# Kernel tuning notes

Measured on AMD Instinct MI355X. Metric: run time of the kernel, lower is better.

Reference implementation:

```python
import jax, jax.numpy as jnp
import numpy as np

TAU_U = 1.0
TAU_L = 0.05
EPS = 1e-12  # torch F.normalize eps


def setup_inputs() -> dict:
    key = jax.random.key(0)
    ks = jax.random.split(key, 8)
    N, D, B = 100000, 128, 8192
    x1 = jax.random.normal(ks[0], (N, D), dtype=jnp.float32)
    x2 = jax.random.normal(ks[1], (N, D), dtype=jnp.float32)
    x1_index = jax.random.randint(ks[2], (B,), 0, N, dtype=jnp.int64 if jax.config.jax_enable_x64 else jnp.int32)
    x2_index = jax.random.randint(ks[3], (B,), 0, N, dtype=jnp.int64 if jax.config.jax_enable_x64 else jnp.int32)
    # Linear params (torch Linear default init: U(-1/sqrt(fan_in), 1/sqrt(fan_in)))
    lim1 = 1.0 / np.sqrt(D)
    W1 = jax.random.uniform(ks[4], (D, D), minval=-lim1, maxval=lim1, dtype=jnp.float32)
    b1 = jax.random.uniform(ks[5], (D,), minval=-lim1, maxval=lim1, dtype=jnp.float32)
    W2 = jax.random.uniform(ks[6], (1, D), minval=-lim1, maxval=lim1, dtype=jnp.float32)
    b2 = jax.random.uniform(ks[7], (1,), minval=-lim1, maxval=lim1, dtype=jnp.float32)
    return {"x1": x1, "x2": x2, "x1_index": x1_index, "x2_index": x2_index,
            "W1": W1, "b1": b1, "W2": W2, "b2": b2}


def _l2norm(x):
    # matches torch F.normalize(dim=1) for 2-D input
    n = jnp.sqrt(jnp.sum(x * x, axis=-1, keepdims=True))
    return x / jnp.maximum(n, EPS)


def reference(x1, x2, x1_index, x2_index, W1, b1, W2, b2):
    x1_feat = _l2norm(x1[x1_index])          # [B, D]
    x2_feat = _l2norm(x2[x2_index])          # [B, D]

    h = x1_feat * x2_feat                    # [B, D]
    h = h @ W1.T + b1                        # lin1
    h = jnp.where(h >= 0, h, 0.2 * h)        # leaky_relu(0.2)
    s = jax.nn.sigmoid(h @ W2.T + b2)        # [B, 1]
    ssl_temp = (TAU_U - TAU_L) * (1.0 - s) + TAU_L   # [B, 1]

    pos = jnp.sum(x1_feat * x2_feat, axis=-1)         # [B]
    # NOTE: [B] / [B,1] broadcasts to [B,B] exactly like torch
    pos_rating = jnp.exp(pos / ssl_temp)              # [B, B]

    tot = x1_feat @ x2_feat.T                          # [B, B]
    tot_rating = jnp.sum(jnp.exp(tot / ssl_temp), axis=1)  # [B]

    ssl_temp_avg = jnp.mean(ssl_temp)
    return (pos_rating, tot_rating, ssl_temp_avg)
```

## Files before the change

kernel.cpp:

```cpp
#include <hip/hip_runtime.h>
#include <stdint.h>

typedef __bf16 bf16x8 __attribute__((ext_vector_type(8)));
typedef float f32x4 __attribute__((ext_vector_type(4)));
typedef __attribute__((address_space(3))) uint32_t as3u32;
typedef const __attribute__((address_space(1))) uint32_t as1u32;

#define B_TOT 8192
#define DD 128
#define OUT_TOT 67108864UL
#define OUT_AVG 67117056UL

__device__ inline unsigned short f2bf(float x){
  union { float f; uint32_t u; } v; v.f = x;
  return (unsigned short)((v.u + 0x7fffu + ((v.u >> 16) & 1u)) >> 16);
}

__device__ inline float bsum128(float v, volatile float* s2){
  #pragma unroll
  for (int o = 32; o; o >>= 1) v += __shfl_xor(v, o);
  __syncthreads();
  if ((threadIdx.x & 63) == 0) s2[threadIdx.x >> 6] = v;
  __syncthreads();
  return s2[0] + s2[1];
}

__global__ __launch_bounds__(128) void k_feat(const float* __restrict__ x1,
    const float* __restrict__ x2, const int* __restrict__ i1a, const int* __restrict__ i2a,
    unsigned short* __restrict__ f1b, unsigned short* __restrict__ f2b,
    unsigned short* __restrict__ hb, float* __restrict__ posw){
  __shared__ float s2[2];
  int b = blockIdx.x, t = threadIdx.x;
  size_t r1 = (size_t)i1a[b] * DD, r2 = (size_t)i2a[b] * DD;
  float v1 = x1[r1 + t], v2 = x2[r2 + t];
  float n1 = sqrtf(bsum128(v1 * v1, s2));
  float f1 = v1 / fmaxf(n1, 1e-12f);
  float n2 = sqrtf(bsum128(v2 * v2, s2));
  float f2 = v2 / fmaxf(n2, 1e-12f);
  float h = f1 * f2;
  float pos = bsum128(h, s2);
  int o = b * DD + t;
  f1b[o] = f2bf(f1); f2b[o] = f2bf(f2); hb[o] = f2bf(h);
  if (t == 0) posw[b] = pos;
}

__device__ inline void stage_tile(const unsigned short* g, unsigned short* s){
  int tid = threadIdx.x;
  #pragma unroll
  for (int it = 0; it < 8; ++it){
    int c = tid + it * 256;
    int row = c >> 4, cc = c & 15;
    int src = (row << 4) + (cc ^ (row & 7));
    __builtin_amdgcn_global_load_lds((as1u32*)(g + src * 8),
                                     (as3u32*)(s + c * 8), 16, 0, 0);
  }
}

__device__ inline void mfma_tile(const unsigned short* As, const unsigned short* Bs,
                                 f32x4 acc[4][4]){
  int tid = threadIdx.x;
  int w = tid >> 6, l = tid & 63;
  int wr = (w >> 1) * 64, wc = (w & 1) * 64;
  int lo = l & 15, hi = l >> 4;
  f32x4 zero = {0.f, 0.f, 0.f, 0.f};
  #pragma unroll
  for (int m = 0; m < 4; ++m)
    #pragma unroll
    for (int n = 0; n < 4; ++n) acc[m][n] = zero;
  #pragma unroll
  for (int kk = 0; kk < 4; ++kk){
    bf16x8 af[4], bfv[4];
    #pragma unroll
    for (int m = 0; m < 4; ++m){
      int row = wr + m * 16 + lo;
      af[m] = *(const bf16x8*)(As + row * 128 + ((kk * 4 + hi) ^ (row & 7)) * 8);
    }
    #pragma unroll
    for (int n = 0; n < 4; ++n){
      int row = wc + n * 16 + lo;
      bfv[n] = *(const bf16x8*)(Bs + row * 128 + ((kk * 4 + hi) ^ (row & 7)) * 8);
    }
    #pragma unroll
    for (int m = 0; m < 4; ++m)
      #pragma unroll
      for (int n = 0; n < 4; ++n)
        acc[m][n] = __builtin_amdgcn_mfma_f32_16x16x32_bf16(af[m], bfv[n], acc[m][n], 0, 0, 0);
  }
}

__global__ __launch_bounds__(256) void k_lin(const unsigned short* __restrict__ hb,
    const float* __restrict__ W1, const float* __restrict__ b1,
    const float* __restrict__ W2, const float* __restrict__ b2,
    float* __restrict__ Tw, float* __restrict__ rTw, float* __restrict__ Tpart){
  __shared__ __align__(16) unsigned short As[16384];
  __shared__ __align__(16) unsigned short Bs[16384];
  __shared__ float zpart[2][128];
  __shared__ float s4[4];
  int i0 = blockIdx.x * 128;
  int tid = threadIdx.x;
  stage_tile(hb + (size_t)i0 * 128, As);
  #pragma unroll
  for (int it = 0; it < 8; ++it){
    int c = tid + it * 256;
    int row = c >> 4, cc = c & 15;
    int src = (row << 4) + (cc ^ (row & 7));
    const float4* g4 = (const float4*)(W1 + src * 8);
    float4 a = g4[0], b = g4[1];
    unsigned short t8[8];
    t8[0] = f2bf(a.x); t8[1] = f2bf(a.y); t8[2] = f2bf(a.z); t8[3] = f2bf(a.w);
    t8[4] = f2bf(b.x); t8[5] = f2bf(b.y); t8[6] = f2bf(b.z); t8[7] = f2bf(b.w);
    *(uint4*)(Bs + c * 8) = *(uint4*)t8;
  }
  asm volatile("s_waitcnt vmcnt(0)" ::: "memory");
  __syncthreads();
  f32x4 acc[4][4];
  mfma_tile(As, Bs, acc);
  int w = tid >> 6, l = tid & 63;
  int wrb = (w >> 1) * 64, wcb = (w & 1) * 64, lo = l & 15, hi = l >> 4;
  float w2v[4], b1v[4];
  #pragma unroll
  for (int n = 0; n < 4; ++n){ int col = wcb + n * 16 + lo; w2v[n] = W2[col]; b1v[n] = b1[col]; }
  #pragma unroll
  for (int m = 0; m < 4; ++m){
    #pragma unroll
    for (int q = 0; q < 4; ++q){
      float p = 0.f;
      #pragma unroll
      for (int n = 0; n < 4; ++n){
        float hv = acc[m][n][q] + b1v[n];
        hv = hv >= 0.f ? hv : 0.2f * hv;
        p += hv * w2v[n];
      }
      p += __shfl_xor(p, 1); p += __shfl_xor(p, 2);
      p += __shfl_xor(p, 4); p += __shfl_xor(p, 8);
      if (lo == 0) zpart[w & 1][wrb + m * 16 + hi * 4 + q] = p;
    }
  }
  __syncthreads();
  float Tloc = 0.f;
  if (tid < 128){
    float z = zpart[0][tid] + zpart[1][tid] + b2[0];
    float s = 1.f / (1.f + __expf(-z));
    float T = 0.95f * (1.f - s) + 0.05f;
    Tw[i0 + tid] = T; rTw[i0 + tid] = 1.f / T;
    Tloc = T;
  }
  float v = Tloc;
  #pragma unroll
  for (int o = 32; o; o >>= 1) v += __shfl_xor(v, o);
  if ((tid & 63) == 0) s4[tid >> 6] = v;
  __syncthreads();
  if (tid == 0) Tpart[blockIdx.x] = s4[0] + s4[1] + s4[2] + s4[3];
}

__global__ __launch_bounds__(256) void k_tot(const unsigned short* __restrict__ f1b,
    const unsigned short* __restrict__ f2b, const float* __restrict__ rTw,
    const float* __restrict__ posw, float* __restrict__ totpart,
    float* __restrict__ out){
  __shared__ __align__(16) unsigned short As[16384];
  __shared__ __align__(16) unsigned short Bs[16384];
  __shared__ float rowacc[2][128];
  __shared__ float posS[128];
  __shared__ float rS[128];
  int bx = (blockIdx.x & 7) * 512 + (blockIdx.x >> 3);
  int rt = bx >> 6, ct = bx & 63;
  stage_tile(f1b + (size_t)rt * 16384, As);
  stage_tile(f2b + (size_t)ct * 16384, Bs);
  asm volatile("s_waitcnt vmcnt(0)" ::: "memory");
  __syncthreads();
  f32x4 acc[4][4];
  mfma_tile(As, Bs, acc);
  int tid = threadIdx.x, w = tid >> 6, l = tid & 63;
  int wrb = (w >> 1) * 64, lo = l & 15, hi = l >> 4;
  int i0 = rt * 128;
  if (tid < 128) posS[tid] = posw[ct * 128 + tid];
  else           rS[tid - 128] = rTw[i0 + tid - 128];
  #pragma unroll
  for (int m = 0; m < 4; ++m){
    #pragma unroll
    for (int q = 0; q < 4; ++q){
      int lr = wrb + m * 16 + hi * 4 + q;
      float r = rTw[i0 + lr];
      float p = __expf(acc[m][0][q] * r) + __expf(acc[m][1][q] * r)
              + __expf(acc[m][2][q] * r) + __expf(acc[m][3][q] * r);
      p += __shfl_xor(p, 1); p += __shfl_xor(p, 2);
      p += __shfl_xor(p, 4); p += __shfl_xor(p, 8);
      if (lo == 0) rowacc[w & 1][lr] = p;
    }
  }
  __syncthreads();
  if (tid < 128) totpart[(size_t)ct * B_TOT + i0 + tid] = rowacc[0][tid] + rowacc[1][tid];
  int c0 = (tid & 31) * 4;
  f32x4 p4 = *(const f32x4*)&posS[c0];
  #pragma unroll
  for (int pass = 0; pass < 16; ++pass){
    int row = pass * 8 + (tid >> 5);
    float r = rS[row];
    f32x4 e;
    e.x = __expf(p4.x * r); e.y = __expf(p4.y * r);
    e.z = __expf(p4.z * r); e.w = __expf(p4.w * r);
    __builtin_nontemporal_store(e, (f32x4*)(out + (size_t)(i0 + row) * B_TOT + ct * 128 + c0));
  }
}

__global__ __launch_bounds__(256) void k_red(const float* __restrict__ totpart,
    const float* __restrict__ Tpart, float* __restrict__ out){
  int i = blockIdx.x * 256 + threadIdx.x;
  float s = 0.f;
  #pragma unroll 8
  for (int ct = 0; ct < 64; ++ct) s += totpart[(size_t)ct * B_TOT + i];
  out[OUT_TOT + i] = s;
  if (blockIdx.x == 0 && threadIdx.x < 64){
    float v = Tpart[threadIdx.x];
    #pragma unroll
    for (int o = 32; o; o >>= 1) v += __shfl_xor(v, o);
    if (threadIdx.x == 0) out[OUT_AVG] = v * (1.0f / 8192.0f);
  }
}

extern "C" void kernel_launch(void* const* d_in, const int* in_sizes, int n_in,
                              void* d_out, int out_size, void* d_ws, size_t ws_size,
                              hipStream_t stream){
  const float* x1 = (const float*)d_in[0];
  const float* x2 = (const float*)d_in[1];
  const int*   i1 = (const int*)d_in[2];
  const int*   i2 = (const int*)d_in[3];
  const float* W1 = (const float*)d_in[4];
  const float* b1 = (const float*)d_in[5];
  const float* W2 = (const float*)d_in[6];
  const float* b2 = (const float*)d_in[7];
  float* out = (float*)d_out;
  char* ws = (char*)d_ws;
  unsigned short* hb   = (unsigned short*)(ws);
  unsigned short* f1b  = (unsigned short*)(ws + 2097152);
  unsigned short* f2b  = (unsigned short*)(ws + 4194304);
  float* posw  = (float*)(ws + 6291456);
  float* Tw    = (float*)(ws + 6324224);
  float* rTw   = (float*)(ws + 6356992);
  float* Tpart = (float*)(ws + 6389760);
  float* totpart = (float*)(ws + 6390016);

  hipLaunchKernelGGL(k_feat,  dim3(8192), dim3(128), 0, stream, x1, x2, i1, i2, f1b, f2b, hb, posw);
  hipLaunchKernelGGL(k_lin,   dim3(64),   dim3(256), 0, stream, hb, W1, b1, W2, b2, Tw, rTw, Tpart);
  hipLaunchKernelGGL(k_tot,   dim3(4096), dim3(256), 0, stream, f1b, f2b, rTw, posw, totpart, out);
  hipLaunchKernelGGL(k_red,   dim3(32),   dim3(256), 0, stream, totpart, Tpart, out);
}
```

Baseline: 100.8 us.

## Replace reduction kernel with atomics and read A fragments directly from global

Removes the final reduction kernel. Row sums of exp(tot/T) are now accumulated into the output with atomicAdd from each tile, and the temperature mean is accumulated atomically from k_lin. The output accumulators are zeroed in k_feat. k_tot no longer stages the A tile into LDS: it loads A fragments straight from global memory, which halves LDS use, and it sets launch bounds to allow 4 blocks per CU. In exchange there are 64 atomic adds per output row, float sums become order-nondeterministic, and the A fragment loads are uncoalesced global reads.

```diff
diff --git a/kernel.cpp b/kernel.cpp
--- a/kernel.cpp
+++ b/kernel.cpp
@@ -28,9 +28,11 @@
 __global__ __launch_bounds__(128) void k_feat(const float* __restrict__ x1,
     const float* __restrict__ x2, const int* __restrict__ i1a, const int* __restrict__ i2a,
     unsigned short* __restrict__ f1b, unsigned short* __restrict__ f2b,
-    unsigned short* __restrict__ hb, float* __restrict__ posw){
+    unsigned short* __restrict__ hb, float* __restrict__ posw, float* __restrict__ out){
   __shared__ float s2[2];
   int b = blockIdx.x, t = threadIdx.x;
+  int gid = b * 128 + t;
+  if (gid <= 8192) out[OUT_TOT + gid] = 0.f;
   size_t r1 = (size_t)i1a[b] * DD, r2 = (size_t)i2a[b] * DD;
   float v1 = x1[r1 + t], v2 = x2[r2 + t];
   float n1 = sqrtf(bsum128(v1 * v1, s2));
@@ -91,7 +93,7 @@
 __global__ __launch_bounds__(256) void k_lin(const unsigned short* __restrict__ hb,
     const float* __restrict__ W1, const float* __restrict__ b1,
     const float* __restrict__ W2, const float* __restrict__ b2,
-    float* __restrict__ Tw, float* __restrict__ rTw, float* __restrict__ Tpart){
+    float* __restrict__ rTw, float* __restrict__ out){
   __shared__ __align__(16) unsigned short As[16384];
   __shared__ __align__(16) unsigned short Bs[16384];
   __shared__ float zpart[2][128];
@@ -142,7 +144,7 @@
     float z = zpart[0][tid] + zpart[1][tid] + b2[0];
     float s = 1.f / (1.f + __expf(-z));
     float T = 0.95f * (1.f - s) + 0.05f;
-    Tw[i0 + tid] = T; rTw[i0 + tid] = 1.f / T;
+    rTw[i0 + tid] = 1.f / T;
     Tloc = T;
   }
   float v = Tloc;
@@ -150,37 +152,59 @@
   for (int o = 32; o; o >>= 1) v += __shfl_xor(v, o);
   if ((tid & 63) == 0) s4[tid >> 6] = v;
   __syncthreads();
-  if (tid == 0) Tpart[blockIdx.x] = s4[0] + s4[1] + s4[2] + s4[3];
-}
-
-__global__ __launch_bounds__(256) void k_tot(const unsigned short* __restrict__ f1b,
+  if (tid == 0) atomicAdd(out + OUT_AVG, (s4[0] + s4[1] + s4[2] + s4[3]) * (1.0f / 8192.0f));
+}
+
+__global__ __launch_bounds__(256, 4) void k_tot(const unsigned short* __restrict__ f1b,
     const unsigned short* __restrict__ f2b, const float* __restrict__ rTw,
-    const float* __restrict__ posw, float* __restrict__ totpart,
-    float* __restrict__ out){
-  __shared__ __align__(16) unsigned short As[16384];
+    const float* __restrict__ posw, float* __restrict__ out){
   __shared__ __align__(16) unsigned short Bs[16384];
   __shared__ float rowacc[2][128];
   __shared__ float posS[128];
   __shared__ float rS[128];
   int bx = (blockIdx.x & 7) * 512 + (blockIdx.x >> 3);
   int rt = bx >> 6, ct = bx & 63;
-  stage_tile(f1b + (size_t)rt * 16384, As);
+  int tid = threadIdx.x, w = tid >> 6, l = tid & 63;
+  int wr = (w >> 1) * 64, wc = (w & 1) * 64;
+  int lo = l & 15, hi = l >> 4;
   stage_tile(f2b + (size_t)ct * 16384, Bs);
+  if (tid < 128) posS[tid] = posw[ct * 128 + tid];
+  else           rS[tid - 128] = rTw[rt * 128 + tid - 128];
+  const unsigned short* Ag = f1b + (size_t)rt * 16384;
+  f32x4 acc[4][4];
+  f32x4 zero = {0.f, 0.f, 0.f, 0.f};
+  #pragma unroll
+  for (int m = 0; m < 4; ++m)
+    #pragma unroll
+    for (int n = 0; n < 4; ++n) acc[m][n] = zero;
   asm volatile("s_waitcnt vmcnt(0)" ::: "memory");
   __syncthreads();
-  f32x4 acc[4][4];
-  mfma_tile(As, Bs, acc);
-  int tid = threadIdx.x, w = tid >> 6, l = tid & 63;
-  int wrb = (w >> 1) * 64, lo = l & 15, hi = l >> 4;
-  int i0 = rt * 128;
-  if (tid < 128) posS[tid] = posw[ct * 128 + tid];
-  else           rS[tid - 128] = rTw[i0 + tid - 128];
+  #pragma unroll
+  for (int kk = 0; kk < 4; ++kk){
+    bf16x8 af[4], bfv[4];
+    #pragma unroll
+    for (int m = 0; m < 4; ++m){
+      int row = wr + m * 16 + lo;
+      af[m] = *(const bf16x8*)(Ag + row * 128 + (kk * 4 + hi) * 8);
+    }
+    #pragma unroll
+    for (int n = 0; n < 4; ++n){
+      int row = wc + n * 16 + lo;
+      bfv[n] = *(const bf16x8*)(Bs + row * 128 + ((kk * 4 + hi) ^ (row & 7)) * 8);
+    }
+    #pragma unroll
+    for (int m = 0; m < 4; ++m)
+      #pragma unroll
+      for (int n = 0; n < 4; ++n)
+        acc[m][n] = __builtin_amdgcn_mfma_f32_16x16x32_bf16(af[m], bfv[n], acc[m][n], 0, 0, 0);
+  }
+  int wrb = wr;
   #pragma unroll
   for (int m = 0; m < 4; ++m){
     #pragma unroll
     for (int q = 0; q < 4; ++q){
       int lr = wrb + m * 16 + hi * 4 + q;
-      float r = rTw[i0 + lr];
+      float r = rS[lr];
       float p = __expf(acc[m][0][q] * r) + __expf(acc[m][1][q] * r)
               + __expf(acc[m][2][q] * r) + __expf(acc[m][3][q] * r);
       p += __shfl_xor(p, 1); p += __shfl_xor(p, 2);
@@ -189,7 +213,7 @@
     }
   }
   __syncthreads();
-  if (tid < 128) totpart[(size_t)ct * B_TOT + i0 + tid] = rowacc[0][tid] + rowacc[1][tid];
+  if (tid < 128) atomicAdd(out + OUT_TOT + rt * 128 + tid, rowacc[0][tid] + rowacc[1][tid]);
   int c0 = (tid & 31) * 4;
   f32x4 p4 = *(const f32x4*)&posS[c0];
   #pragma unroll
@@ -199,22 +223,7 @@
     f32x4 e;
     e.x = __expf(p4.x * r); e.y = __expf(p4.y * r);
     e.z = __expf(p4.z * r); e.w = __expf(p4.w * r);
-    __builtin_nontemporal_store(e, (f32x4*)(out + (size_t)(i0 + row) * B_TOT + ct * 128 + c0));
-  }
-}
-
-__global__ __launch_bounds__(256) void k_red(const float* __restrict__ totpart,
-    const float* __restrict__ Tpart, float* __restrict__ out){
-  int i = blockIdx.x * 256 + threadIdx.x;
-  float s = 0.f;
-  #pragma unroll 8
-  for (int ct = 0; ct < 64; ++ct) s += totpart[(size_t)ct * B_TOT + i];
-  out[OUT_TOT + i] = s;
-  if (blockIdx.x == 0 && threadIdx.x < 64){
-    float v = Tpart[threadIdx.x];
-    #pragma unroll
-    for (int o = 32; o; o >>= 1) v += __shfl_xor(v, o);
-    if (threadIdx.x == 0) out[OUT_AVG] = v * (1.0f / 8192.0f);
+    __builtin_nontemporal_store(e, (f32x4*)(out + (size_t)(rt * 128 + row) * B_TOT + ct * 128 + c0));
   }
 }
 
@@ -235,13 +244,9 @@
   unsigned short* f1b  = (unsigned short*)(ws + 2097152);
   unsigned short* f2b  = (unsigned short*)(ws + 4194304);
   float* posw  = (float*)(ws + 6291456);
-  float* Tw    = (float*)(ws + 6324224);
-  float* rTw   = (float*)(ws + 6356992);
-  float* Tpart = (float*)(ws + 6389760);
-  float* totpart = (float*)(ws + 6390016);
-
-  hipLaunchKernelGGL(k_feat,  dim3(8192), dim3(128), 0, stream, x1, x2, i1, i2, f1b, f2b, hb, posw);
-  hipLaunchKernelGGL(k_lin,   dim3(64),   dim3(256), 0, stream, hb, W1, b1, W2, b2, Tw, rTw, Tpart);
-  hipLaunchKernelGGL(k_tot,   dim3(4096), dim3(256), 0, stream, f1b, f2b, rTw, posw, totpart, out);
-  hipLaunchKernelGGL(k_red,   dim3(32),   dim3(256), 0, stream, totpart, Tpart, out);
-}
+  float* rTw   = (float*)(ws + 6324224);
+
+  hipLaunchKernelGGL(k_feat,  dim3(8192), dim3(128), 0, stream, x1, x2, i1, i2, f1b, f2b, hb, posw, out);
+  hipLaunchKernelGGL(k_lin,   dim3(64),   dim3(256), 0, stream, hb, W1, b1, W2, b2, rTw, out);
+  hipLaunchKernelGGL(k_tot,   dim3(4096), dim3(256), 0, stream, f1b, f2b, rTw, posw, out);
+}
```

After: 95.36 us. -5.4%, faster.
